# Optimization experiments

Hardware: AMD Instinct MI355X
Metric: run time of the kernel (lower is better)

Reference implementation:

```python
import math
import jax, jax.numpy as jnp
import numpy as np

N_HEAD = 16

def rms_norm(x, w, eps=1e-6):
    x32 = x.astype(jnp.float32)
    ms = jnp.mean(x32 * x32, axis=-1, keepdims=True)
    y = (x32 * jax.lax.rsqrt(ms + eps)).astype(x.dtype)
    return y * w

def apply_rope(x, cos, sin):
    # x: [B,H,S,D], cos/sin: [S,D/2] broadcast over B,H
    half = x.shape[-1] // 2
    x1, x2 = x[..., :half], x[..., half:]
    return jnp.concatenate((x1 * cos - x2 * sin, x2 * cos + x1 * sin), axis=-1).astype(x.dtype)

def setup_inputs() -> dict:
    key = jax.random.key(0)
    ks = jax.random.split(key, 8)
    B, S, D = 1, 4096, 1024
    hd = D // N_HEAD
    x = jax.random.normal(ks[0], (B, S, D), dtype=jnp.float32)
    # rotary embeddings
    inv_freq = 1.0 / (10000.0 ** (jnp.arange(0, hd, 2, dtype=jnp.float32) / hd))  # [hd/2]
    ang = jnp.arange(S, dtype=jnp.float32)[:, None] * inv_freq  # [S, hd/2]
    cos, sin = jnp.cos(ang), jnp.sin(ang)
    # additive causal mask [1,1,S,S]
    causal = jnp.tril(jnp.ones((S, S), dtype=bool))
    attention_mask = jnp.where(causal, 0.0, -1e9).astype(jnp.float32)[None, None]
    init = 0.02
    wq = jax.random.normal(ks[1], (D, D), dtype=jnp.float32) * init
    wk = jax.random.normal(ks[2], (D, D), dtype=jnp.float32) * init
    wv = jax.random.normal(ks[3], (D, D), dtype=jnp.float32) * init
    wo = jax.random.normal(ks[4], (D, D), dtype=jnp.float32) * init
    q_norm_w = jnp.ones((hd,), dtype=jnp.float32)
    k_norm_w = jnp.ones((hd,), dtype=jnp.float32)
    return {"x": x, "cos": cos, "sin": sin, "attention_mask": attention_mask,
            "wq": wq, "wk": wk, "wv": wv, "wo": wo,
            "q_norm_w": q_norm_w, "k_norm_w": k_norm_w}

def reference(x, cos, sin, attention_mask, wq, wk, wv, wo, q_norm_w, k_norm_w):
    B, S, D = x.shape
    H = N_HEAD
    hd = D // H
    q = (x @ wq.T).reshape(B, S, H, hd)
    k = (x @ wk.T).reshape(B, S, H, hd)
    v = (x @ wv.T).reshape(B, S, H, hd)
    q = jnp.swapaxes(rms_norm(q, q_norm_w), 1, 2)  # [B,H,S,hd]
    k = jnp.swapaxes(rms_norm(k, k_norm_w), 1, 2)
    v = jnp.swapaxes(v, 1, 2)
    q = apply_rope(q, cos, sin)
    k = apply_rope(k, cos, sin)
    scores = jnp.einsum('bhqd,bhkd->bhqk', q, k) / math.sqrt(hd)
    scores = scores + attention_mask
    attn = jax.nn.softmax(scores.astype(jnp.float32), axis=-1).astype(q.dtype)
    o = jnp.einsum('bhqk,bhkd->bhqd', attn, v)  # [B,H,S,hd]
    o = jnp.swapaxes(o, 1, 2).reshape(B, S, D)
    return o @ wo.T
```

## Files before the change

kernel.cpp:

```cpp
#include <hip/hip_runtime.h>

#define S_LEN 4096
#define DIM   1024
#define NH    16
#define HD    64

typedef __bf16 bf16;
typedef __attribute__((ext_vector_type(8)))  __bf16 bf16x8;
typedef __attribute__((ext_vector_type(4)))  float  f32x4;
typedef __attribute__((ext_vector_type(16))) float  f32x16;
typedef __attribute__((ext_vector_type(4)))  unsigned int uint4v;

typedef __attribute__((address_space(3))) void lds_void;
typedef __attribute__((address_space(1))) void g_void;

#if __has_builtin(__builtin_amdgcn_exp2f)
#define EXP2(x) __builtin_amdgcn_exp2f(x)
#else
#define EXP2(x) exp2f(x)
#endif

__device__ __forceinline__ void gl_lds16(const void* g, void* l) {
    __builtin_amdgcn_global_load_lds((g_void*)(void*)g, (lds_void*)l, 16, 0, 0);
}

__device__ __forceinline__ unsigned int pk2(float a, float b) {
    unsigned short ua = __builtin_bit_cast(unsigned short, (bf16)a);
    unsigned short ub = __builtin_bit_cast(unsigned short, (bf16)b);
    return (unsigned int)ua | ((unsigned int)ub << 16);
}

__device__ __forceinline__ int ksw23(int x) {
    return (x & ~12) | ((x & 8) >> 1) | ((x & 4) << 1);
}

__global__ __launch_bounds__(256) void f2b_all(
    const float* __restrict__ x,  const float* __restrict__ wq,
    const float* __restrict__ wk, const float* __restrict__ wv,
    const float* __restrict__ wo,
    bf16* __restrict__ xb, bf16* __restrict__ wqkv, bf16* __restrict__ wob)
{
    int b = blockIdx.x;
    const float* src; bf16* dst; int base;
    if (b < 2048)      { src = x;  dst = xb;              base = b; }
    else if (b < 2560) { src = wq; dst = wqkv;            base = b - 2048; }
    else if (b < 3072) { src = wk; dst = wqkv + 1048576;  base = b - 2560; }
    else if (b < 3584) { src = wv; dst = wqkv + 2097152;  base = b - 3072; }
    else               { src = wo; dst = wob;             base = b - 3584; }
    int i = base * 2048 + threadIdx.x * 8;
    float4 a = *(const float4*)(src + i);
    float4 c = *(const float4*)(src + i + 4);
    bf16x8 r;
    r[0]=(bf16)a.x; r[1]=(bf16)a.y; r[2]=(bf16)a.z; r[3]=(bf16)a.w;
    r[4]=(bf16)c.x; r[5]=(bf16)c.y; r[6]=(bf16)c.z; r[7]=(bf16)c.w;
    *(bf16x8*)(dst + i) = r;
}

template <int MODE>
__global__ __launch_bounds__(256) void gemm_bt(
    const bf16* __restrict__ A, const bf16* __restrict__ B,
    int M, int N, int K,
    float* __restrict__ outF,
    bf16* __restrict__ outQ, bf16* __restrict__ outK, bf16* __restrict__ outV)
{
    __shared__ bf16 As[128][32];
    __shared__ bf16 Bs[128][32];
    const int bm = blockIdx.x, bn = blockIdx.y;
    const int tid  = threadIdx.x;
    const int wave = tid >> 6, lane = tid & 63;
    const int g = lane >> 4, r = lane & 15;
    const int wr = wave >> 1, wc = wave & 1;
    const int rr = lane >> 2, cc = (lane & 3) * 8;

    f32x4 acc[4][4] = {};

    const bf16* Ab = A + (size_t)(bm * 128) * K;
    const bf16* Bb = B + (size_t)(bn * 128) * K;

    for (int k0 = 0; k0 < K; k0 += 32) {
        #pragma unroll
        for (int i = 0; i < 2; ++i) {
            gl_lds16(Ab + (size_t)(wave*32 + i*16 + rr) * K + k0 + cc, &As[wave*32 + i*16][0]);
            gl_lds16(Bb + (size_t)(wave*32 + i*16 + rr) * K + k0 + cc, &Bs[wave*32 + i*16][0]);
        }
        __syncthreads();
        bf16x8 a[4], b[4];
        #pragma unroll
        for (int m = 0; m < 4; ++m) a[m] = *(const bf16x8*)&As[wr*64 + m*16 + r][g*8];
        #pragma unroll
        for (int n = 0; n < 4; ++n) b[n] = *(const bf16x8*)&Bs[wc*64 + n*16 + r][g*8];
        #pragma unroll
        for (int m = 0; m < 4; ++m)
            #pragma unroll
            for (int n = 0; n < 4; ++n)
                acc[m][n] = __builtin_amdgcn_mfma_f32_16x16x32_bf16(a[m], b[n], acc[m][n], 0, 0, 0);
        __syncthreads();
    }

    #pragma unroll
    for (int m = 0; m < 4; ++m)
        #pragma unroll
        for (int n = 0; n < 4; ++n)
            #pragma unroll
            for (int i = 0; i < 4; ++i) {
                int row = bm*128 + wr*64 + m*16 + g*4 + i;
                int col = bn*128 + wc*64 + n*16 + r;
                float val = acc[m][n][i];
                if (MODE == 0) {
                    outF[(size_t)row * N + col] = val;
                } else {
                    if (col < 1024)       outQ[(size_t)row * 1024 + col]          = (bf16)val;
                    else if (col < 2048)  outK[(size_t)row * 1024 + (col - 1024)] = (bf16)val;
                    else {
                        int c = col - 2048;
                        int hh = c >> 6, d = c & 63;
                        int pos = ksw23(row & 63) ^ ((d & 7) << 3);
                        outV[((size_t)(hh * HD + d)) * S_LEN + (row & ~63) + pos] = (bf16)val;
                    }
                }
            }
}

__global__ __launch_bounds__(256) void norm_rope(
    const bf16* __restrict__ qr, const bf16* __restrict__ kr,
    const float* __restrict__ cosb, const float* __restrict__ sinb,
    const float* __restrict__ qw, const float* __restrict__ kw,
    bf16* __restrict__ qo, bf16* __restrict__ ko)
{
    int wgl  = blockIdx.x * 4 + (threadIdx.x >> 6);
    int lane = threadIdx.x & 63;
    int isK  = wgl >= 8192;
    int w2   = wgl & 8191;
    int s    = w2 >> 1;
    int h    = ((w2 & 1) << 3) + (lane >> 3);
    int d0   = (lane & 7) << 3;
    const bf16*  src = isK ? kr : qr;
    const float* w   = isK ? kw : qw;

    bf16x8 xv = *(const bf16x8*)(src + (size_t)s * DIM + h * HD + d0);
    float x[8];
    #pragma unroll
    for (int e = 0; e < 8; ++e) x[e] = (float)xv[e];
    float ss = 0.f;
    #pragma unroll
    for (int e = 0; e < 8; ++e) ss += x[e] * x[e];
    ss += __shfl_xor(ss, 1);
    ss += __shfl_xor(ss, 2);
    ss += __shfl_xor(ss, 4);
    float rn = rsqrtf(ss * (1.0f / 64.0f) + 1e-6f);

    float4 w0 = *(const float4*)(w + d0);
    float4 w1 = *(const float4*)(w + d0 + 4);
    float wv[8] = {w0.x, w0.y, w0.z, w0.w, w1.x, w1.y, w1.z, w1.w};
    float xn[8], pr[8];
    #pragma unroll
    for (int e = 0; e < 8; ++e) xn[e] = x[e] * rn * wv[e];
    #pragma unroll
    for (int e = 0; e < 8; ++e) pr[e] = __shfl_xor(xn[e], 4);

    int dm = d0 & 31;
    float4 c0 = *(const float4*)(cosb + s * 32 + dm);
    float4 c1 = *(const float4*)(cosb + s * 32 + dm + 4);
    float4 sn0 = *(const float4*)(sinb + s * 32 + dm);
    float4 sn1 = *(const float4*)(sinb + s * 32 + dm + 4);
    float cv[8] = {c0.x, c0.y, c0.z, c0.w, c1.x, c1.y, c1.z, c1.w};
    float sv[8] = {sn0.x, sn0.y, sn0.z, sn0.w, sn1.x, sn1.y, sn1.z, sn1.w};

    const bool lo = (d0 < 32);
    bf16x8 y;
    #pragma unroll
    for (int e = 0; e < 8; ++e) {
        float t = lo ? (xn[e] * cv[e] - pr[e] * sv[e])
                     : (xn[e] * cv[e] + pr[e] * sv[e]);
        y[e] = (bf16)t;
    }
    size_t ob = ((size_t)h * S_LEN + s) * HD;
    if (isK) *(bf16x8*)(ko + ob + (d0 ^ ((s & 7) << 3))) = y;
    else     *(bf16x8*)(qo + ob + d0)                    = y;
}

__global__ __launch_bounds__(256, 4) void attn_kernel(
    const bf16* __restrict__ q, const bf16* __restrict__ k,
    const bf16* __restrict__ vt,
    bf16* __restrict__ Opc, float* __restrict__ lpc)
{
    __shared__ bf16 Ks[2][64][64];
    __shared__ bf16 Vt[2][64][64];

    const int idx = blockIdx.x;
    const int h = idx & 15;
    const int u = idx >> 4;
    const int qt = 31 - (u >> 2);
    const int c  = u & 3;
    const int nt = 2 * qt + 2;
    const int t0 = (c * nt) >> 2;
    const int t1 = ((c + 1) * nt) >> 2;

    const int q0 = qt * 128;
    const int tid = threadIdx.x;
    const int wave = tid >> 6, lane = tid & 63;
    const int l31 = lane & 31, hi = lane >> 5;

    const bf16* qh  = q  + (size_t)h * S_LEN * HD;
    const bf16* kh  = k  + (size_t)h * S_LEN * HD;
    const bf16* vth = vt + (size_t)h * HD * S_LEN;

    const int qrow = q0 + wave * 32 + l31;
    bf16x8 qf[4];
    #pragma unroll
    for (int ds4 = 0; ds4 < 4; ++ds4)
        qf[ds4] = *(const bf16x8*)(qh + (size_t)qrow * HD + ds4 * 16 + hi * 8);

    float l_run = 0.f;
    f32x16 acc_o[2] = {};

    const int srow = lane >> 3, scol = (lane & 7) * 8;
    const float C1 = 0.125f * 1.44269504088896f;
    const float C2 = 8.0f * 1.44269504088896f;

    auto stage = [&](int t, int buf) {
        const int k0 = t * 64;
        const bf16* kb = kh + (size_t)(k0 + wave * 16) * HD;
        gl_lds16(kb + (size_t)(srow    ) * HD + scol, &Ks[buf][wave * 16][0]);
        gl_lds16(kb + (size_t)(srow + 8) * HD + scol, &Ks[buf][wave * 16 + 8][0]);
        const bf16* vb = vth + (size_t)(wave * 16) * S_LEN + k0;
        gl_lds16(vb + (size_t)(srow    ) * S_LEN + scol, &Vt[buf][wave * 16][0]);
        gl_lds16(vb + (size_t)(srow + 8) * S_LEN + scol, &Vt[buf][wave * 16 + 8][0]);
    };

#define COMPUTE_TILE(T, BUF)                                                  \
    do {                                                                      \
        const int k0_ = (T) * 64;                                             \
        const bool masked_ = ((T) >= 2 * qt);                                 \
        f32x16 sacc_[2];                                                      \
        __builtin_amdgcn_s_setprio(1);                                        \
        _Pragma("unroll")                                                     \
        for (int kn = 0; kn < 2; ++kn) {                                      \
            const int krow = kn * 32 + l31;                                   \
            const int sw = (krow & 7) << 3;                                   \
            f32x16 z = {};                                                    \
            _Pragma("unroll")                                                 \
            for (int ds4 = 0; ds4 < 4; ++ds4) {                               \
                bf16x8 kfr = *(const bf16x8*)&Ks[BUF][krow][(ds4 * 16 + hi * 8) ^ sw]; \
                z = __builtin_amdgcn_mfma_f32_32x32x16_bf16(kfr, qf[ds4], z, 0, 0, 0); \
            }                                                                 \
            sacc_[kn] = z;                                                    \
        }                                                                     \
        __builtin_amdgcn_s_setprio(0);                                        \
        float p_[32];                                                         \
        _Pragma("unroll")                                                     \
        for (int kn = 0; kn < 2; ++kn)                                        \
            _Pragma("unroll")                                                 \
            for (int rg = 0; rg < 16; ++rg) {                                 \
                float e = EXP2(fmaf(sacc_[kn][rg], C1, -C2));                 \
                if (masked_) {                                                \
                    int kloc = kn * 32 + (rg & 3) + 8 * (rg >> 2) + 4 * hi;   \
                    if (k0_ + kloc > qrow) e = 0.f;                           \
                }                                                             \
                p_[kn * 16 + rg] = e;                                         \
            }                                                                 \
        float s0_ = 0.f, s1_ = 0.f, s2_ = 0.f, s3_ = 0.f;                     \
        _Pragma("unroll")                                                     \
        for (int j = 0; j < 8; ++j) {                                         \
            s0_ += p_[4*j];   s1_ += p_[4*j+1];                               \
            s2_ += p_[4*j+2]; s3_ += p_[4*j+3];                               \
        }                                                                     \
        float rs_ = (s0_ + s1_) + (s2_ + s3_);                                \
        rs_ += __shfl_xor(rs_, 32);                                           \
        l_run += rs_;                                                         \
        bf16x8 pa_[4];                                                        \
        _Pragma("unroll")                                                     \
        for (int ks4 = 0; ks4 < 4; ++ks4) {                                   \
            uint4v w_;                                                        \
            w_.x = pk2(p_[8*ks4+0], p_[8*ks4+1]);                             \
            w_.y = pk2(p_[8*ks4+2], p_[8*ks4+3]);                             \
            w_.z = pk2(p_[8*ks4+4], p_[8*ks4+5]);                             \
            w_.w = pk2(p_[8*ks4+6], p_[8*ks4+7]);                             \
            pa_[ks4] = __builtin_bit_cast(bf16x8, w_);                        \
        }                                                                     \
        __builtin_amdgcn_s_setprio(1);                                        \
        _Pragma("unroll")                                                     \
        for (int n = 0; n < 2; ++n) {                                         \
            const int d = n * 32 + l31;                                       \
            const int sw = (d & 7) << 3;                                      \
            f32x16 a = acc_o[n];                                              \
            _Pragma("unroll")                                                 \
            for (int ks4 = 0; ks4 < 4; ++ks4) {                               \
                bf16x8 vfr = *(const bf16x8*)&Vt[BUF][d][(ks4 * 16 + hi * 8) ^ sw]; \
                a = __builtin_amdgcn_mfma_f32_32x32x16_bf16(pa_[ks4], vfr, a, 0, 0, 0); \
            }                                                                 \
            acc_o[n] = a;                                                     \
        }                                                                     \
        __builtin_amdgcn_s_setprio(0);                                        \
    } while (0)

    if (t0 < t1) {
        stage(t0, 0);
        asm volatile("s_waitcnt vmcnt(0)" ::: "memory");
        __syncthreads();
        int t = t0;
        while (t + 2 <= t1) {
            stage(t + 1, 1);
            COMPUTE_TILE(t, 0);
            asm volatile("s_waitcnt vmcnt(0)" ::: "memory");
            __syncthreads();
            if (t + 2 < t1) stage(t + 2, 0);
            COMPUTE_TILE(t + 1, 1);
            asm volatile("s_waitcnt vmcnt(0)" ::: "memory");
            __syncthreads();
            t += 2;
        }
        if (t < t1) COMPUTE_TILE(t, 0);
    }
#undef COMPUTE_TILE

    bf16* Op = Opc + (size_t)c * S_LEN * DIM;
    #pragma unroll
    for (int n = 0; n < 2; ++n)
        #pragma unroll
        for (int rg = 0; rg < 16; ++rg) {
            int s_abs = q0 + wave * 32 + (rg & 3) + 8 * (rg >> 2) + 4 * hi;
            Op[(size_t)s_abs * DIM + h * HD + n * 32 + l31] = (bf16)acc_o[n][rg];
        }
    if (lane < 32)
        lpc[c * (NH * S_LEN) + h * S_LEN + (q0 + wave * 32 + lane)] = l_run;
}

__global__ __launch_bounds__(256) void combine_kernel(
    const bf16* __restrict__ Opc, const float* __restrict__ lpc,
    bf16* __restrict__ o)
{
    int gid = blockIdx.x * 256 + threadIdx.x;
    int e = gid * 8;
    int s = e >> 10, h = (e & 1023) >> 6;
    float a[8] = {};
    #pragma unroll
    for (int c = 0; c < 4; ++c) {
        bf16x8 v = *(const bf16x8*)(Opc + (size_t)c * S_LEN * DIM + e);
        #pragma unroll
        for (int j = 0; j < 8; ++j) a[j] += (float)v[j];
    }
    float l = 0.f;
    #pragma unroll
    for (int c = 0; c < 4; ++c) l += lpc[c * (NH * S_LEN) + h * S_LEN + s];
    float inv = __builtin_amdgcn_rcpf(l);
    bf16x8 rv;
    #pragma unroll
    for (int j = 0; j < 8; ++j) rv[j] = (bf16)(a[j] * inv);
    *(bf16x8*)(o + e) = rv;
}

extern "C" void kernel_launch(void* const* d_in, const int* in_sizes, int n_in,
                              void* d_out, int out_size, void* d_ws, size_t ws_size,
                              hipStream_t stream)
{
    const float* x    = (const float*)d_in[0];
    const float* cosb = (const float*)d_in[1];
    const float* sinb = (const float*)d_in[2];
    const float* wq   = (const float*)d_in[4];
    const float* wk   = (const float*)d_in[5];
    const float* wv   = (const float*)d_in[6];
    const float* wo   = (const float*)d_in[7];
    const float* qw   = (const float*)d_in[8];
    const float* kw   = (const float*)d_in[9];

    char* ws = (char*)d_ws;
    const size_t MB = 1024 * 1024;
    bf16*  wob   = (bf16*)(ws + 0);
    bf16*  xb    = (bf16*)(ws + 2 * MB);
    bf16*  q_ws  = (bf16*)(ws + 2 * MB);
    bf16*  o_ws  = (bf16*)(ws + 2 * MB);
    bf16*  wqkv  = (bf16*)(ws + 10 * MB);
    bf16*  k_ws  = (bf16*)(ws + 10 * MB);
    bf16*  q_raw = (bf16*)(ws + 18 * MB);
    bf16*  k_raw = (bf16*)(ws + 26 * MB);
    bf16*  Opc   = (bf16*)(ws + 18 * MB);
    bf16*  vt_ws = (bf16*)(ws + 50 * MB);
    float* lpc   = (float*)(ws + 58 * MB);

    f2b_all<<<4096, 256, 0, stream>>>(x, wq, wk, wv, wo, xb, wqkv, wob);

    gemm_bt<1><<<dim3(32, 24), 256, 0, stream>>>(xb, wqkv, 4096, 3072, 1024,
                                                 nullptr, q_raw, k_raw, vt_ws);
    norm_rope<<<4096, 256, 0, stream>>>(q_raw, k_raw, cosb, sinb,
                                        qw, kw, q_ws, k_ws);
    attn_kernel<<<2048, 256, 0, stream>>>(q_ws, k_ws, vt_ws, Opc, lpc);
    combine_kernel<<<4096 * 1024 / 8 / 256, 256, 0, stream>>>(Opc, lpc, o_ws);
    gemm_bt<0><<<dim3(32, 8), 256, 0, stream>>>(o_ws, wob, 4096, 1024, 1024,
                                                (float*)d_out, nullptr, nullptr, nullptr);
}
```

Baseline: 149.8 us.

## Fuse QK RMSNorm and RoPE into QKV GEMM epilogue, drop norm_rope kernel

Moves the per-head RMSNorm and rotary embedding into the QKV projection GEMM's epilogue, using cross-lane shuffles to reduce over each head's 64 columns and pairing MFMA tiles for the rotation. This removes the separate norm_rope launch and the intermediate raw Q/K write and re-read. The epilogue now does scalar bf16 stores and extra cos/sin loads, which may coalesce less well. The attention kernel's launch bound is also raised to 5 waves per SIMD, which may increase register pressure.

Result: slower. 190.4 us (+27.1%).

```diff
diff --git a/kernel.cpp b/kernel.cpp
--- a/kernel.cpp
+++ b/kernel.cpp
@@ -61,7 +61,9 @@
     const bf16* __restrict__ A, const bf16* __restrict__ B,
     int M, int N, int K,
     float* __restrict__ outF,
-    bf16* __restrict__ outQ, bf16* __restrict__ outK, bf16* __restrict__ outV)
+    bf16* __restrict__ outQ, bf16* __restrict__ outK, bf16* __restrict__ outV,
+    const float* __restrict__ cosb, const float* __restrict__ sinb,
+    const float* __restrict__ qw,   const float* __restrict__ kw)
 {
     __shared__ bf16 As[128][32];
     __shared__ bf16 Bs[128][32];
@@ -97,89 +99,79 @@
         __syncthreads();
     }
 
-    #pragma unroll
-    for (int m = 0; m < 4; ++m)
-        #pragma unroll
-        for (int n = 0; n < 4; ++n)
+    if (MODE == 0) {
+        #pragma unroll
+        for (int m = 0; m < 4; ++m)
+            #pragma unroll
+            for (int n = 0; n < 4; ++n)
+                #pragma unroll
+                for (int i = 0; i < 4; ++i) {
+                    int row = bm*128 + wr*64 + m*16 + g*4 + i;
+                    int col = bn*128 + wc*64 + n*16 + r;
+                    outF[(size_t)row * N + col] = acc[m][n][i];
+                }
+    } else if (bn >= 16) {
+        #pragma unroll
+        for (int m = 0; m < 4; ++m)
+            #pragma unroll
+            for (int n = 0; n < 4; ++n)
+                #pragma unroll
+                for (int i = 0; i < 4; ++i) {
+                    int row = bm*128 + wr*64 + m*16 + g*4 + i;
+                    int col = bn*128 + wc*64 + n*16 + r;
+                    int c2 = col - 2048;
+                    int hh = c2 >> 6, d = c2 & 63;
+                    int pos = ksw23(row & 63) ^ ((d & 7) << 3);
+                    outV[((size_t)(hh * HD + d)) * S_LEN + (row & ~63) + pos] = (bf16)acc[m][n][i];
+                }
+    } else {
+        const bool isK = (bn >= 8);
+        const float* wn = isK ? kw : qw;
+        bf16* dst = isK ? outK : outQ;
+        const int h = ((bn & 7) << 1) | wc;
+        float wv4[4];
+        #pragma unroll
+        for (int n = 0; n < 4; ++n) wv4[n] = wn[n * 16 + r];
+        #pragma unroll
+        for (int m = 0; m < 4; ++m)
             #pragma unroll
             for (int i = 0; i < 4; ++i) {
-                int row = bm*128 + wr*64 + m*16 + g*4 + i;
-                int col = bn*128 + wc*64 + n*16 + r;
-                float val = acc[m][n][i];
-                if (MODE == 0) {
-                    outF[(size_t)row * N + col] = val;
+                int srow = bm*128 + wr*64 + m*16 + g*4 + i;
+                float ss = acc[m][0][i]*acc[m][0][i] + acc[m][1][i]*acc[m][1][i]
+                         + acc[m][2][i]*acc[m][2][i] + acc[m][3][i]*acc[m][3][i];
+                ss += __shfl_xor(ss, 1);
+                ss += __shfl_xor(ss, 2);
+                ss += __shfl_xor(ss, 4);
+                ss += __shfl_xor(ss, 8);
+                float rn = rsqrtf(ss * (1.0f / 64.0f) + 1e-6f);
+                float xn0 = acc[m][0][i] * rn * wv4[0];
+                float xn1 = acc[m][1][i] * rn * wv4[1];
+                float xn2 = acc[m][2][i] * rn * wv4[2];
+                float xn3 = acc[m][3][i] * rn * wv4[3];
+                float c0 = cosb[srow * 32 + r],      c1 = cosb[srow * 32 + 16 + r];
+                float s0 = sinb[srow * 32 + r],      s1 = sinb[srow * 32 + 16 + r];
+                float y0 = xn0 * c0 - xn2 * s0;
+                float y1 = xn1 * c1 - xn3 * s1;
+                float y2 = xn2 * c0 + xn0 * s0;
+                float y3 = xn3 * c1 + xn1 * s1;
+                size_t ob = ((size_t)h * S_LEN + srow) * HD;
+                if (isK) {
+                    int sw = (srow & 7) << 3;
+                    dst[ob + ((     r) ^ sw)] = (bf16)y0;
+                    dst[ob + ((16 + r) ^ sw)] = (bf16)y1;
+                    dst[ob + ((32 + r) ^ sw)] = (bf16)y2;
+                    dst[ob + ((48 + r) ^ sw)] = (bf16)y3;
                 } else {
-                    if (col < 1024)       outQ[(size_t)row * 1024 + col]          = (bf16)val;
-                    else if (col < 2048)  outK[(size_t)row * 1024 + (col - 1024)] = (bf16)val;
-                    else {
-                        int c = col - 2048;
-                        int hh = c >> 6, d = c & 63;
-                        int pos = ksw23(row & 63) ^ ((d & 7) << 3);
-                        outV[((size_t)(hh * HD + d)) * S_LEN + (row & ~63) + pos] = (bf16)val;
-                    }
+                    dst[ob +      r] = (bf16)y0;
+                    dst[ob + 16 + r] = (bf16)y1;
+                    dst[ob + 32 + r] = (bf16)y2;
+                    dst[ob + 48 + r] = (bf16)y3;
                 }
             }
-}
-
-__global__ __launch_bounds__(256) void norm_rope(
-    const bf16* __restrict__ qr, const bf16* __restrict__ kr,
-    const float* __restrict__ cosb, const float* __restrict__ sinb,
-    const float* __restrict__ qw, const float* __restrict__ kw,
-    bf16* __restrict__ qo, bf16* __restrict__ ko)
-{
-    int wgl  = blockIdx.x * 4 + (threadIdx.x >> 6);
-    int lane = threadIdx.x & 63;
-    int isK  = wgl >= 8192;
-    int w2   = wgl & 8191;
-    int s    = w2 >> 1;
-    int h    = ((w2 & 1) << 3) + (lane >> 3);
-    int d0   = (lane & 7) << 3;
-    const bf16*  src = isK ? kr : qr;
-    const float* w   = isK ? kw : qw;
-
-    bf16x8 xv = *(const bf16x8*)(src + (size_t)s * DIM + h * HD + d0);
-    float x[8];
-    #pragma unroll
-    for (int e = 0; e < 8; ++e) x[e] = (float)xv[e];
-    float ss = 0.f;
-    #pragma unroll
-    for (int e = 0; e < 8; ++e) ss += x[e] * x[e];
-    ss += __shfl_xor(ss, 1);
-    ss += __shfl_xor(ss, 2);
-    ss += __shfl_xor(ss, 4);
-    float rn = rsqrtf(ss * (1.0f / 64.0f) + 1e-6f);
-
-    float4 w0 = *(const float4*)(w + d0);
-    float4 w1 = *(const float4*)(w + d0 + 4);
-    float wv[8] = {w0.x, w0.y, w0.z, w0.w, w1.x, w1.y, w1.z, w1.w};
-    float xn[8], pr[8];
-    #pragma unroll
-    for (int e = 0; e < 8; ++e) xn[e] = x[e] * rn * wv[e];
-    #pragma unroll
-    for (int e = 0; e < 8; ++e) pr[e] = __shfl_xor(xn[e], 4);
-
-    int dm = d0 & 31;
-    float4 c0 = *(const float4*)(cosb + s * 32 + dm);
-    float4 c1 = *(const float4*)(cosb + s * 32 + dm + 4);
-    float4 sn0 = *(const float4*)(sinb + s * 32 + dm);
-    float4 sn1 = *(const float4*)(sinb + s * 32 + dm + 4);
-    float cv[8] = {c0.x, c0.y, c0.z, c0.w, c1.x, c1.y, c1.z, c1.w};
-    float sv[8] = {sn0.x, sn0.y, sn0.z, sn0.w, sn1.x, sn1.y, sn1.z, sn1.w};
-
-    const bool lo = (d0 < 32);
-    bf16x8 y;
-    #pragma unroll
-    for (int e = 0; e < 8; ++e) {
-        float t = lo ? (xn[e] * cv[e] - pr[e] * sv[e])
-                     : (xn[e] * cv[e] + pr[e] * sv[e]);
-        y[e] = (bf16)t;
     }
-    size_t ob = ((size_t)h * S_LEN + s) * HD;
-    if (isK) *(bf16x8*)(ko + ob + (d0 ^ ((s & 7) << 3))) = y;
-    else     *(bf16x8*)(qo + ob + d0)                    = y;
-}
-
-__global__ __launch_bounds__(256, 4) void attn_kernel(
+}
+
+__global__ __launch_bounds__(256, 5) void attn_kernel(
     const bf16* __restrict__ q, const bf16* __restrict__ k,
     const bf16* __restrict__ vt,
     bf16* __restrict__ Opc, float* __restrict__ lpc)
@@ -367,25 +359,23 @@
     char* ws = (char*)d_ws;
     const size_t MB = 1024 * 1024;
     bf16*  wob   = (bf16*)(ws + 0);
-    bf16*  xb    = (bf16*)(ws + 2 * MB);
     bf16*  q_ws  = (bf16*)(ws + 2 * MB);
-    bf16*  o_ws  = (bf16*)(ws + 2 * MB);
-    bf16*  wqkv  = (bf16*)(ws + 10 * MB);
     bf16*  k_ws  = (bf16*)(ws + 10 * MB);
-    bf16*  q_raw = (bf16*)(ws + 18 * MB);
-    bf16*  k_raw = (bf16*)(ws + 26 * MB);
-    bf16*  Opc   = (bf16*)(ws + 18 * MB);
-    bf16*  vt_ws = (bf16*)(ws + 50 * MB);
+    bf16*  vt_ws = (bf16*)(ws + 18 * MB);
+    bf16*  Opc   = (bf16*)(ws + 26 * MB);
+    bf16*  o_ws  = (bf16*)(ws + 26 * MB);
+    bf16*  xb    = (bf16*)(ws + 26 * MB);
+    bf16*  wqkv  = (bf16*)(ws + 34 * MB);
     float* lpc   = (float*)(ws + 58 * MB);
 
     f2b_all<<<4096, 256, 0, stream>>>(x, wq, wk, wv, wo, xb, wqkv, wob);
 
     gemm_bt<1><<<dim3(32, 24), 256, 0, stream>>>(xb, wqkv, 4096, 3072, 1024,
-                                                 nullptr, q_raw, k_raw, vt_ws);
-    norm_rope<<<4096, 256, 0, stream>>>(q_raw, k_raw, cosb, sinb,
-                                        qw, kw, q_ws, k_ws);
+                                                 nullptr, q_ws, k_ws, vt_ws,
+                                                 cosb, sinb, qw, kw);
     attn_kernel<<<2048, 256, 0, stream>>>(q_ws, k_ws, vt_ws, Opc, lpc);
     combine_kernel<<<4096 * 1024 / 8 / 256, 256, 0, stream>>>(Opc, lpc, o_ws);
     gemm_bt<0><<<dim3(32, 8), 256, 0, stream>>>(o_ws, wob, 4096, 1024, 1024,
-                                                (float*)d_out, nullptr, nullptr, nullptr);
-}
+                                                (float*)d_out, nullptr, nullptr, nullptr,
+                                                nullptr, nullptr, nullptr, nullptr);
+}
```
